# Optimization experiments

Hardware: AMD Instinct MI355X
Metric: run time of the kernel (lower is better)

## Reference

```python
import jax, jax.numpy as jnp
import numpy as np

EMBED_DIM = 1024
N_HEADS = 16
HEAD_DIM = EMBED_DIM // N_HEADS
SEQ_LEN = 4096


def setup_inputs() -> dict:
    key = jax.random.key(0)
    k1, k2 = jax.random.split(key)
    x = jax.random.normal(k1, (SEQ_LEN, EMBED_DIM), dtype=jnp.float32)
    # Linear params (lecun-normal-ish scale)
    W_qkv = jax.random.normal(k2, (EMBED_DIM, 3 * EMBED_DIM), dtype=jnp.float32) / np.sqrt(EMBED_DIM)
    b_qkv = jnp.zeros((3 * EMBED_DIM,), dtype=jnp.float32)
    return {"x": x, "W_qkv": W_qkv, "b_qkv": b_qkv}


def reference(x, W_qkv, b_qkv):
    T = x.shape[0]
    # Fused QKV projection: [T, 3*E]
    qkv = x @ W_qkv + b_qkv
    q, k, v = jnp.split(qkv, 3, axis=-1)
    # [T, N, H]
    q = q.reshape(T, N_HEADS, HEAD_DIM)
    k = k.reshape(T, N_HEADS, HEAD_DIM)
    v = v.reshape(T, N_HEADS, HEAD_DIM)
    # Standard SDPA (module does NOT pass is_causal, so full attention)
    scale = 1.0 / np.sqrt(HEAD_DIM).astype(np.float32)
    logits = jnp.einsum("qnh,knh->nqk", q, k) * scale  # [N, T, T]
    attn = jax.nn.softmax(logits, axis=-1)
    y = jnp.einsum("nqk,knh->qnh", attn, v)  # [T, N, H]
    return y
```

## Files before the change

### kernel.cpp

```cpp
#include <hip/hip_runtime.h>

#define T_SEQ 4096
#define EMB   1024
#define NH    16
#define HD    64
#define N3    3072

#define SCL2 0.18033688011112042f

using u16 = unsigned short;
using u32 = unsigned int;
typedef __bf16 bf16x8 __attribute__((ext_vector_type(8)));
typedef float  f32x4  __attribute__((ext_vector_type(4)));
typedef float  f32x16 __attribute__((ext_vector_type(16)));
typedef u16    u16x8  __attribute__((ext_vector_type(8)));

#if __has_builtin(__builtin_amdgcn_exp2f)
#define EXP2(x) __builtin_amdgcn_exp2f(x)
#else
#define EXP2(x) exp2f(x)
#endif

__device__ inline u16 f2bf(float f) {
    union { float f; unsigned u; } v; v.f = f;
    unsigned u = v.u;
    u += 0x7FFFu + ((u >> 16) & 1u);
    return (u16)(u >> 16);
}

__global__ void convert_x_kernel(const float* __restrict__ x, u16* __restrict__ xb) {
    int i = (blockIdx.x * 256 + threadIdx.x) * 8;
    float4 a = *(const float4*)(x + i);
    float4 b = *(const float4*)(x + i + 4);
    u16x8 o;
    o[0] = f2bf(a.x); o[1] = f2bf(a.y); o[2] = f2bf(a.z); o[3] = f2bf(a.w);
    o[4] = f2bf(b.x); o[5] = f2bf(b.y); o[6] = f2bf(b.z); o[7] = f2bf(b.w);
    *(u16x8*)(xb + i) = o;
}

__global__ void transpose_w_kernel(const float* __restrict__ W, u16* __restrict__ Wt) {
    __shared__ float tile[64][72];
    int n0 = blockIdx.x * 64, k0 = blockIdx.y * 64;
    float qs = (n0 < 1024) ? SCL2 : 1.0f;
    int t = threadIdx.x;
#pragma unroll
    for (int p = 0; p < 16; ++p) {
        int idx = p * 256 + t;
        int r = idx >> 6, c = idx & 63;
        tile[r][c] = W[(k0 + r) * N3 + n0 + c];
    }
    __syncthreads();
    int c2 = t >> 2;
    int kg = (t & 3) * 16;
    u16x8 o0, o1;
#pragma unroll
    for (int j = 0; j < 8; ++j) o0[j] = f2bf(tile[kg + j][c2] * qs);
#pragma unroll
    for (int j = 0; j < 8; ++j) o1[j] = f2bf(tile[kg + 8 + j][c2] * qs);
    u16* dst = Wt + (n0 + c2) * EMB + k0 + kg;
    *(u16x8*)dst = o0;
    *(u16x8*)(dst + 8) = o1;
}

__global__ __launch_bounds__(256) void gemm_qkv_kernel(const u16* __restrict__ xb,
                                                       const u16* __restrict__ Wt,
                                                       const float* __restrict__ bias,
                                                       u16* __restrict__ qkv) {
    __shared__ __align__(16) u16 Alds[128 * 64];
    __shared__ __align__(16) u16 Blds[128 * 64];
    int tid = threadIdx.x;
    int lane = tid & 63, wave = tid >> 6;
    int wm = wave >> 1, wn = wave & 1;
    int m0 = blockIdx.y * 128, n0 = blockIdx.x * 128;
    int lr = lane & 15, lg = lane >> 4;

    f32x4 acc[4][4] = {};

    for (int kt = 0; kt < 16; ++kt) {
        int kbase = kt * 64;
#pragma unroll
        for (int p = 0; p < 4; ++p) {
            int g = p * 256 + tid;
            int row = g >> 3;
            int cg = (g & 7) << 3;
            int sg = (((cg >> 3) ^ (row & 7)) << 3);
            u16x8 va = *(const u16x8*)(xb + (m0 + row) * EMB + kbase + cg);
            *(u16x8*)&Alds[row * 64 + sg] = va;
            u16x8 vb = *(const u16x8*)(Wt + (n0 + row) * EMB + kbase + cg);
            *(u16x8*)&Blds[row * 64 + sg] = vb;
        }
        __syncthreads();
#pragma unroll
        for (int ks = 0; ks < 2; ++ks) {
            bf16x8 af[4], bf[4];
#pragma unroll
            for (int mi = 0; mi < 4; ++mi) {
                int row = wm * 64 + mi * 16 + lr;
                int sg = ((ks * 4 + lg) ^ (row & 7)) << 3;
                af[mi] = *(const bf16x8*)&Alds[row * 64 + sg];
            }
#pragma unroll
            for (int ni = 0; ni < 4; ++ni) {
                int row = wn * 64 + ni * 16 + lr;
                int sg = ((ks * 4 + lg) ^ (row & 7)) << 3;
                bf[ni] = *(const bf16x8*)&Blds[row * 64 + sg];
            }
#pragma unroll
            for (int mi = 0; mi < 4; ++mi)
#pragma unroll
                for (int ni = 0; ni < 4; ++ni)
                    acc[mi][ni] = __builtin_amdgcn_mfma_f32_16x16x32_bf16(af[mi], bf[ni], acc[mi][ni], 0, 0, 0);
        }
        __syncthreads();
    }
#pragma unroll
    for (int ni = 0; ni < 4; ++ni) {
        int n = n0 + wn * 64 + ni * 16 + lr;
        float bv = bias[n];
        if (n < 1024) bv *= SCL2;
#pragma unroll
        for (int mi = 0; mi < 4; ++mi) {
            int mrow = m0 + wm * 64 + mi * 16 + lg * 4;
#pragma unroll
            for (int r = 0; r < 4; ++r)
                qkv[(mrow + r) * N3 + n] = f2bf(acc[mi][ni][r] + bv);
        }
    }
}

__global__ void transpose_v_kernel(const u16* __restrict__ qkv, u16* __restrict__ Vt) {
    __shared__ u16 tile[64][72];
    int c0 = blockIdx.x * 64;
    int t0 = blockIdx.y * 64;
    int t = threadIdx.x;
#pragma unroll
    for (int p = 0; p < 16; ++p) {
        int idx = p * 256 + t;
        int r = idx >> 6, c = idx & 63;
        tile[r][c] = qkv[(t0 + r) * N3 + 2048 + c0 + c];
    }
    __syncthreads();
    int c2 = t >> 2;
    int kg = (t & 3) * 16;
    u16x8 o0, o1;
#pragma unroll
    for (int j = 0; j < 8; ++j) o0[j] = tile[kg + j][c2];
#pragma unroll
    for (int j = 0; j < 8; ++j) o1[j] = tile[kg + 8 + j][c2];
    u16* dst = Vt + (c0 + c2) * T_SEQ + t0 + kg;
    *(u16x8*)dst = o0;
    *(u16x8*)(dst + 8) = o1;
}

__device__ inline u32 cvtpk(float lo, float hi) {
    u32 r;
    asm("v_cvt_pk_bf16_f32 %0, %1, %2" : "=v"(r) : "v"(lo), "v"(hi));
    return r;
}

__device__ inline bf16x8 mk8(u32 w0, u32 w1, u32 w2, u32 w3) {
    union { u32 w[4]; bf16x8 v; } u;
    u.w[0] = w0; u.w[1] = w1; u.w[2] = w2; u.w[3] = w3;
    return u.v;
}

__device__ inline float vsum16(f32x16 v) {
    float a0 = v[0] + v[1],  a1 = v[2] + v[3];
    float a2 = v[4] + v[5],  a3 = v[6] + v[7];
    float a4 = v[8] + v[9],  a5 = v[10] + v[11];
    float a6 = v[12] + v[13], a7 = v[14] + v[15];
    float b0 = a0 + a1, b1 = a2 + a3, b2 = a4 + a5, b3 = a6 + a7;
    return (b0 + b1) + (b2 + b3);
}

__device__ inline void pack2(f32x16 p, int hi, bf16x8& fe, bf16x8& fo) {
    u32 a0 = cvtpk(p[0], p[1]),   a1 = cvtpk(p[2], p[3]);
    u32 a2 = cvtpk(p[4], p[5]),   a3 = cvtpk(p[6], p[7]);
    u32 b0 = cvtpk(p[8], p[9]),   b1 = cvtpk(p[10], p[11]);
    u32 b2 = cvtpk(p[12], p[13]), b3 = cvtpk(p[14], p[15]);
    u32 xa0 = (u32)__shfl_xor((int)a0, 32), xa1 = (u32)__shfl_xor((int)a1, 32);
    u32 xa2 = (u32)__shfl_xor((int)a2, 32), xa3 = (u32)__shfl_xor((int)a3, 32);
    u32 xb0 = (u32)__shfl_xor((int)b0, 32), xb1 = (u32)__shfl_xor((int)b1, 32);
    u32 xb2 = (u32)__shfl_xor((int)b2, 32), xb3 = (u32)__shfl_xor((int)b3, 32);
    fe = hi ? mk8(xa2, xa3, a2, a3) : mk8(a0, a1, xa0, xa1);
    fo = hi ? mk8(xb2, xb3, b2, b3) : mk8(b0, b1, xb0, xb1);
}

#define KVROW 72

__global__ __launch_bounds__(256, 2) void attn_kernel(const u16* __restrict__ qkv,
                                                      const u16* __restrict__ Vt,
                                                      float* __restrict__ out) {
    __shared__ __align__(16) char smem[73728];

    int tid = threadIdx.x, lane = tid & 63, wave = tid >> 6;
    int ql = lane & 31, hi = lane >> 5;
    int g = wave >> 1;
    int wq = wave & 1;
    int tid2 = tid & 127;
    int h = blockIdx.y;
    int q0 = blockIdx.x * 128;

    char* base = smem + g * 36864;
    u16* K0 = (u16*)base;
    u16* V0 = (u16*)(base + 9216);
    u16* K1 = (u16*)(base + 18432);
    u16* V1 = (u16*)(base + 27648);

    bf16x8 qfA[4], qfB[4];
    {
        const u16* qpA = qkv + (size_t)(q0 + wq * 64 + ql) * N3 + h * HD;
        const u16* qpB = qpA + (size_t)32 * N3;
#pragma unroll
        for (int c = 0; c < 4; ++c) {
            qfA[c] = *(const bf16x8*)(qpA + c * 16 + hi * 8);
            qfB[c] = *(const bf16x8*)(qpB + c * 16 + hi * 8);
        }
    }

    f32x16 accA0 = {}, accA1 = {}, accB0 = {}, accB1 = {};
    float lrA = 0.f, lrB = 0.f;

    int srow = (tid2 >> 3) & 15, spg = tid2 & 7;
    const u16* kptr = qkv + (size_t)(g * 2048) * N3 + EMB + h * HD;
    const u16* vptr = Vt + (size_t)(h * HD) * T_SEQ + g * 2048;

    u16x8 kstg[4], vstg[4];
#pragma unroll
    for (int j = 0; j < 4; ++j) {
        kstg[j] = *(const u16x8*)(kptr + (size_t)(srow + 16 * j) * N3 + spg * 8);
        vstg[j] = *(const u16x8*)(vptr + (size_t)(srow + 16 * j) * T_SEQ + spg * 8);
    }

    int koff = ql * KVROW + hi * 8;

    for (int t = 0; t < 32; ++t) {
        u16* Kl = (t & 1) ? K1 : K0;
        u16* Vl = (t & 1) ? V1 : V0;
#pragma unroll
        for (int j = 0; j < 4; ++j) {
            *(u16x8*)&Kl[(srow + 16 * j) * KVROW + spg * 8] = kstg[j];
            *(u16x8*)&Vl[(srow + 16 * j) * KVROW + spg * 8] = vstg[j];
        }
        if (t < 31) {
            const u16* kb = kptr + (size_t)(t + 1) * 64 * N3;
            const u16* vb = vptr + (t + 1) * 64;
#pragma unroll
            for (int j = 0; j < 4; ++j) {
                kstg[j] = *(const u16x8*)(kb + (size_t)(srow + 16 * j) * N3 + spg * 8);
                vstg[j] = *(const u16x8*)(vb + (size_t)(srow + 16 * j) * T_SEQ + spg * 8);
            }
        }
        __syncthreads();

        f32x16 sA0 = {}, sA1 = {}, sB0 = {}, sB1 = {};
#pragma unroll
        for (int c = 0; c < 4; ++c) {
            bf16x8 kf = *(const bf16x8*)&Kl[koff + c * 16];
            sA0 = __builtin_amdgcn_mfma_f32_32x32x16_bf16(kf, qfA[c], sA0, 0, 0, 0);
            sB0 = __builtin_amdgcn_mfma_f32_32x32x16_bf16(kf, qfB[c], sB0, 0, 0, 0);
        }
#pragma unroll
        for (int c = 0; c < 4; ++c) {
            bf16x8 kf = *(const bf16x8*)&Kl[koff + 32 * KVROW + c * 16];
            sA1 = __builtin_amdgcn_mfma_f32_32x32x16_bf16(kf, qfA[c], sA1, 0, 0, 0);
            sB1 = __builtin_amdgcn_mfma_f32_32x32x16_bf16(kf, qfB[c], sB1, 0, 0, 0);
        }

#pragma unroll
        for (int r = 0; r < 16; ++r) sA0[r] = EXP2(sA0[r]);
#pragma unroll
        for (int r = 0; r < 16; ++r) sA1[r] = EXP2(sA1[r]);
#pragma unroll
        for (int r = 0; r < 16; ++r) sB0[r] = EXP2(sB0[r]);
#pragma unroll
        for (int r = 0; r < 16; ++r) sB1[r] = EXP2(sB1[r]);

        {
            float sa = vsum16(sA0) + vsum16(sA1);
            sa += __shfl_xor(sa, 32);
            lrA += sa;
            float sb = vsum16(sB0) + vsum16(sB1);
            sb += __shfl_xor(sb, 32);
            lrB += sb;
        }

        bf16x8 paA0, paA1, paA2, paA3, paB0, paB1, paB2, paB3;
        pack2(sA0, hi, paA0, paA1);
        pack2(sA1, hi, paA2, paA3);
        pack2(sB0, hi, paB0, paB1);
        pack2(sB1, hi, paB2, paB3);

#pragma unroll
        for (int c = 0; c < 4; ++c) {
            bf16x8 pbA = (c == 0) ? paA0 : (c == 1) ? paA1 : (c == 2) ? paA2 : paA3;
            bf16x8 pbB = (c == 0) ? paB0 : (c == 1) ? paB1 : (c == 2) ? paB2 : paB3;
            bf16x8 vf0 = *(const bf16x8*)&Vl[koff + c * 16];
            accA0 = __builtin_amdgcn_mfma_f32_32x32x16_bf16(vf0, pbA, accA0, 0, 0, 0);
            accB0 = __builtin_amdgcn_mfma_f32_32x32x16_bf16(vf0, pbB, accB0, 0, 0, 0);
            bf16x8 vf1 = *(const bf16x8*)&Vl[koff + 32 * KVROW + c * 16];
            accA1 = __builtin_amdgcn_mfma_f32_32x32x16_bf16(vf1, pbA, accA1, 0, 0, 0);
            accB1 = __builtin_amdgcn_mfma_f32_32x32x16_bf16(vf1, pbB, accB1, 0, 0, 0);
        }
    }

    __syncthreads();

    float* Xb = (float*)(smem + 36864);
    float* lX = Xb + 2 * 64 * 68;

    if (g == 1) {
        float* ob = Xb + wq * (64 * 68);
#pragma unroll
        for (int gg = 0; gg < 4; ++gg) {
            int d = 8 * gg + 4 * hi;
            f32x4 a0 = { accA0[4 * gg], accA0[4 * gg + 1], accA0[4 * gg + 2], accA0[4 * gg + 3] };
            *(f32x4*)&ob[ql * 68 + d] = a0;
            f32x4 a1 = { accA1[4 * gg], accA1[4 * gg + 1], accA1[4 * gg + 2], accA1[4 * gg + 3] };
            *(f32x4*)&ob[ql * 68 + 32 + d] = a1;
            f32x4 b0 = { accB0[4 * gg], accB0[4 * gg + 1], accB0[4 * gg + 2], accB0[4 * gg + 3] };
            *(f32x4*)&ob[(32 + ql) * 68 + d] = b0;
            f32x4 b1 = { accB1[4 * gg], accB1[4 * gg + 1], accB1[4 * gg + 2], accB1[4 * gg + 3] };
            *(f32x4*)&ob[(32 + ql) * 68 + 32 + d] = b1;
        }
        if (hi == 0) {
            lX[wq * 64 + ql] = lrA;
            lX[wq * 64 + 32 + ql] = lrB;
        }
    }
    __syncthreads();

    if (g == 0) {
        float* ob = Xb + wq * (64 * 68);
        float invA = 1.0f / (lrA + lX[wq * 64 + ql]);
        float invB = 1.0f / (lrB + lX[wq * 64 + 32 + ql]);
        float* tb = (float*)smem + wq * (64 * 68);
#pragma unroll
        for (int gg = 0; gg < 4; ++gg) {
            int d = 8 * gg + 4 * hi;
            f32x4 xa0 = *(const f32x4*)&ob[ql * 68 + d];
            f32x4 wa0 = { (accA0[4 * gg] + xa0[0]) * invA, (accA0[4 * gg + 1] + xa0[1]) * invA,
                          (accA0[4 * gg + 2] + xa0[2]) * invA, (accA0[4 * gg + 3] + xa0[3]) * invA };
            *(f32x4*)&tb[ql * 68 + d] = wa0;
            f32x4 xa1 = *(const f32x4*)&ob[ql * 68 + 32 + d];
            f32x4 wa1 = { (accA1[4 * gg] + xa1[0]) * invA, (accA1[4 * gg + 1] + xa1[1]) * invA,
                          (accA1[4 * gg + 2] + xa1[2]) * invA, (accA1[4 * gg + 3] + xa1[3]) * invA };
            *(f32x4*)&tb[ql * 68 + 32 + d] = wa1;
            f32x4 xb0 = *(const f32x4*)&ob[(32 + ql) * 68 + d];
            f32x4 wb0 = { (accB0[4 * gg] + xb0[0]) * invB, (accB0[4 * gg + 1] + xb0[1]) * invB,
                          (accB0[4 * gg + 2] + xb0[2]) * invB, (accB0[4 * gg + 3] + xb0[3]) * invB };
            *(f32x4*)&tb[(32 + ql) * 68 + d] = wb0;
            f32x4 xb1 = *(const f32x4*)&ob[(32 + ql) * 68 + 32 + d];
            f32x4 wb1 = { (accB1[4 * gg] + xb1[0]) * invB, (accB1[4 * gg + 1] + xb1[1]) * invB,
                          (accB1[4 * gg + 2] + xb1[2]) * invB, (accB1[4 * gg + 3] + xb1[3]) * invB };
            *(f32x4*)&tb[(32 + ql) * 68 + 32 + d] = wb1;
        }
    }
    __syncthreads();

    if (g == 0) {
        float* tb = (float*)smem + wq * (64 * 68);
#pragma unroll
        for (int qq = 0; qq < 16; ++qq) {
            int q = qq * 4 + (lane >> 4);
            int d4 = (lane & 15) * 4;
            f32x4 v = *(const f32x4*)&tb[q * 68 + d4];
            *(f32x4*)&out[(size_t)(q0 + wq * 64 + q) * EMB + h * HD + d4] = v;
        }
    }
}

extern "C" void kernel_launch(void* const* d_in, const int* in_sizes, int n_in,
                              void* d_out, int out_size, void* d_ws, size_t ws_size,
                              hipStream_t stream) {
    (void)in_sizes; (void)n_in; (void)out_size; (void)ws_size;
    const float* x = (const float*)d_in[0];
    const float* W = (const float*)d_in[1];
    const float* b = (const float*)d_in[2];
    float* out = (float*)d_out;

    u16* xb  = (u16*)d_ws;
    u16* Wt  = xb  + (size_t)T_SEQ * EMB;
    u16* qkv = Wt  + (size_t)N3 * EMB;
    u16* Vt  = qkv + (size_t)T_SEQ * N3;

    convert_x_kernel<<<(T_SEQ * EMB) / (256 * 8), 256, 0, stream>>>(x, xb);
    transpose_w_kernel<<<dim3(N3 / 64, EMB / 64), 256, 0, stream>>>(W, Wt);
    gemm_qkv_kernel<<<dim3(N3 / 128, T_SEQ / 128), 256, 0, stream>>>(xb, Wt, b, qkv);
    transpose_v_kernel<<<dim3(EMB / 64, T_SEQ / 64), 256, 0, stream>>>(qkv, Vt);
    attn_kernel<<<dim3(T_SEQ / 128, NH), 256, 0, stream>>>(qkv, Vt, out);
}
```

Baseline: 162.5 us.

## Fuse V transpose into QKV GEMM epilogue and relax attention launch bounds

The GEMM epilogue now writes the V third of the projection directly in transposed layout (Vt) using 4-element vector stores, so the separate transpose_v kernel and its read/write pass over V are removed. The attention kernel's launch bounds drop from 2 to 1 minimum blocks per CU, which gives the compiler more register budget but may lower occupancy. MFMA calls are also wrapped in a macro, which is cosmetic. The transposed stores are strided across rows, so write coalescing in the epilogue may be worse than before.

```diff
diff --git a/kernel.cpp b/kernel.cpp
--- a/kernel.cpp
+++ b/kernel.cpp
@@ -13,6 +13,7 @@
 typedef __bf16 bf16x8 __attribute__((ext_vector_type(8)));
 typedef float  f32x4  __attribute__((ext_vector_type(4)));
 typedef float  f32x16 __attribute__((ext_vector_type(16)));
+typedef u16    u16x4  __attribute__((ext_vector_type(4)));
 typedef u16    u16x8  __attribute__((ext_vector_type(8)));
 
 #if __has_builtin(__builtin_amdgcn_exp2f)
@@ -20,6 +21,8 @@
 #else
 #define EXP2(x) exp2f(x)
 #endif
+
+#define MFMA32(a, b, c) __builtin_amdgcn_mfma_f32_32x32x16_bf16((a), (b), (c), 0, 0, 0)
 
 __device__ inline u16 f2bf(float f) {
     union { float f; unsigned u; } v; v.f = f;
@@ -65,7 +68,8 @@
 __global__ __launch_bounds__(256) void gemm_qkv_kernel(const u16* __restrict__ xb,
                                                        const u16* __restrict__ Wt,
                                                        const float* __restrict__ bias,
-                                                       u16* __restrict__ qkv) {
+                                                       u16* __restrict__ qkv,
+                                                       u16* __restrict__ Vt) {
     __shared__ __align__(16) u16 Alds[128 * 64];
     __shared__ __align__(16) u16 Blds[128 * 64];
     int tid = threadIdx.x;
@@ -113,43 +117,36 @@
         }
         __syncthreads();
     }
-#pragma unroll
-    for (int ni = 0; ni < 4; ++ni) {
-        int n = n0 + wn * 64 + ni * 16 + lr;
-        float bv = bias[n];
-        if (n < 1024) bv *= SCL2;
-#pragma unroll
-        for (int mi = 0; mi < 4; ++mi) {
-            int mrow = m0 + wm * 64 + mi * 16 + lg * 4;
-#pragma unroll
-            for (int r = 0; r < 4; ++r)
-                qkv[(mrow + r) * N3 + n] = f2bf(acc[mi][ni][r] + bv);
-        }
-    }
-}
-
-__global__ void transpose_v_kernel(const u16* __restrict__ qkv, u16* __restrict__ Vt) {
-    __shared__ u16 tile[64][72];
-    int c0 = blockIdx.x * 64;
-    int t0 = blockIdx.y * 64;
-    int t = threadIdx.x;
-#pragma unroll
-    for (int p = 0; p < 16; ++p) {
-        int idx = p * 256 + t;
-        int r = idx >> 6, c = idx & 63;
-        tile[r][c] = qkv[(t0 + r) * N3 + 2048 + c0 + c];
-    }
-    __syncthreads();
-    int c2 = t >> 2;
-    int kg = (t & 3) * 16;
-    u16x8 o0, o1;
-#pragma unroll
-    for (int j = 0; j < 8; ++j) o0[j] = tile[kg + j][c2];
-#pragma unroll
-    for (int j = 0; j < 8; ++j) o1[j] = tile[kg + 8 + j][c2];
-    u16* dst = Vt + (c0 + c2) * T_SEQ + t0 + kg;
-    *(u16x8*)dst = o0;
-    *(u16x8*)(dst + 8) = o1;
+    if (n0 < 2048) {
+#pragma unroll
+        for (int ni = 0; ni < 4; ++ni) {
+            int n = n0 + wn * 64 + ni * 16 + lr;
+            float bv = bias[n];
+            if (n < 1024) bv *= SCL2;
+#pragma unroll
+            for (int mi = 0; mi < 4; ++mi) {
+                int mrow = m0 + wm * 64 + mi * 16 + lg * 4;
+#pragma unroll
+                for (int r = 0; r < 4; ++r)
+                    qkv[(mrow + r) * N3 + n] = f2bf(acc[mi][ni][r] + bv);
+            }
+        }
+    } else {
+#pragma unroll
+        for (int ni = 0; ni < 4; ++ni) {
+            int n = n0 + wn * 64 + ni * 16 + lr;
+            float bv = bias[n];
+            int nc = n - 2048;
+#pragma unroll
+            for (int mi = 0; mi < 4; ++mi) {
+                int mrow = m0 + wm * 64 + mi * 16 + lg * 4;
+                u16x4 o;
+#pragma unroll
+                for (int r = 0; r < 4; ++r) o[r] = f2bf(acc[mi][ni][r] + bv);
+                *(u16x4*)&Vt[(size_t)nc * T_SEQ + mrow] = o;
+            }
+        }
+    }
 }
 
 __device__ inline u32 cvtpk(float lo, float hi) {
@@ -188,7 +185,7 @@
 
 #define KVROW 72
 
-__global__ __launch_bounds__(256, 2) void attn_kernel(const u16* __restrict__ qkv,
+__global__ __launch_bounds__(256, 1) void attn_kernel(const u16* __restrict__ qkv,
                                                       const u16* __restrict__ Vt,
                                                       float* __restrict__ out) {
     __shared__ __align__(16) char smem[73728];
@@ -257,14 +254,14 @@
 #pragma unroll
         for (int c = 0; c < 4; ++c) {
             bf16x8 kf = *(const bf16x8*)&Kl[koff + c * 16];
-            sA0 = __builtin_amdgcn_mfma_f32_32x32x16_bf16(kf, qfA[c], sA0, 0, 0, 0);
-            sB0 = __builtin_amdgcn_mfma_f32_32x32x16_bf16(kf, qfB[c], sB0, 0, 0, 0);
+            sA0 = MFMA32(kf, qfA[c], sA0);
+            sB0 = MFMA32(kf, qfB[c], sB0);
         }
 #pragma unroll
         for (int c = 0; c < 4; ++c) {
             bf16x8 kf = *(const bf16x8*)&Kl[koff + 32 * KVROW + c * 16];
-            sA1 = __builtin_amdgcn_mfma_f32_32x32x16_bf16(kf, qfA[c], sA1, 0, 0, 0);
-            sB1 = __builtin_amdgcn_mfma_f32_32x32x16_bf16(kf, qfB[c], sB1, 0, 0, 0);
+            sA1 = MFMA32(kf, qfA[c], sA1);
+            sB1 = MFMA32(kf, qfB[c], sB1);
         }
 
 #pragma unroll
@@ -296,11 +293,11 @@
             bf16x8 pbA = (c == 0) ? paA0 : (c == 1) ? paA1 : (c == 2) ? paA2 : paA3;
             bf16x8 pbB = (c == 0) ? paB0 : (c == 1) ? paB1 : (c == 2) ? paB2 : paB3;
             bf16x8 vf0 = *(const bf16x8*)&Vl[koff + c * 16];
-            accA0 = __builtin_amdgcn_mfma_f32_32x32x16_bf16(vf0, pbA, accA0, 0, 0, 0);
-            accB0 = __builtin_amdgcn_mfma_f32_32x32x16_bf16(vf0, pbB, accB0, 0, 0, 0);
+            accA0 = MFMA32(vf0, pbA, accA0);
+            accB0 = MFMA32(vf0, pbB, accB0);
             bf16x8 vf1 = *(const bf16x8*)&Vl[koff + 32 * KVROW + c * 16];
-            accA1 = __builtin_amdgcn_mfma_f32_32x32x16_bf16(vf1, pbA, accA1, 0, 0, 0);
-            accB1 = __builtin_amdgcn_mfma_f32_32x32x16_bf16(vf1, pbB, accB1, 0, 0, 0);
+            accA1 = MFMA32(vf1, pbA, accA1);
+            accB1 = MFMA32(vf1, pbB, accB1);
         }
     }
 
@@ -386,7 +383,6 @@
 
     convert_x_kernel<<<(T_SEQ * EMB) / (256 * 8), 256, 0, stream>>>(x, xb);
     transpose_w_kernel<<<dim3(N3 / 64, EMB / 64), 256, 0, stream>>>(W, Wt);
-    gemm_qkv_kernel<<<dim3(N3 / 128, T_SEQ / 128), 256, 0, stream>>>(xb, Wt, b, qkv);
-    transpose_v_kernel<<<dim3(EMB / 64, T_SEQ / 64), 256, 0, stream>>>(qkv, Vt);
+    gemm_qkv_kernel<<<dim3(N3 / 128, T_SEQ / 128), 256, 0, stream>>>(xb, Wt, b, qkv, Vt);
     attn_kernel<<<dim3(T_SEQ / 128, NH), 256, 0, stream>>>(qkv, Vt, out);
 }
```

After: 168.5 us. +3.7%, slower.
